# Optimization experiments

Measured on AMD Instinct MI355X. Metric: run time of the kernel, lower is better.

Reference implementation:

```python
import jax, jax.numpy as jnp
import numpy as np

IN_FEATURES = 16080
TREES = 64
LEAVES = 128
CLASSES = 16
BATCH = 64


def setup_inputs() -> dict:
    key = jax.random.key(0)
    k_x, k_w, k_b, k_c = jax.random.split(key, 4)
    x = jax.random.normal(k_x, (BATCH, TREES, IN_FEATURES), dtype=jnp.float32)
    # nn.Linear(16080, leaves): weight [leaves, in], bias [leaves]
    lim = 1.0 / np.sqrt(IN_FEATURES)
    W = jax.random.uniform(k_w, (LEAVES, IN_FEATURES), minval=-lim, maxval=lim, dtype=jnp.float32)
    b = jax.random.uniform(k_b, (LEAVES,), minval=-lim, maxval=lim, dtype=jnp.float32)
    # contribution parameter ~ U(-1, 1), shape [trees, leaves, classes]
    contribution = jax.random.uniform(k_c, (TREES, LEAVES, CLASSES), minval=-1.0, maxval=1.0, dtype=jnp.float32)
    return {"x": x, "W": W, "b": b, "contribution": contribution}


def reference(x, W, b, contribution):
    # Linear + Hardtanh: [B, T, L]
    symbolic_paths = jnp.clip(jnp.einsum('bti,li->btl', x, W) + b, -1.0, 1.0)
    # Fused form of the per-(tree,leaf) outer-product loop: [B, T, L, C]
    class_value = symbolic_paths[..., None] * contribution[None]
    p = jax.nn.softmax(class_value, axis=-1)
    # 1 - sum(p^2) over classes (Gini-style impurity): [B, T, L]
    class_value = jnp.sum(1.0 - p * p, axis=-1)
    return (symbolic_paths, class_value)
```

## Files before the change

kernel.cpp:

```cpp
#include <hip/hip_runtime.h>
#include <hip/hip_bf16.h>
#include <stdint.h>

#define IN_F   16080
#define NTREES 64
#define NLEAF  128
#define NCLS   16
#define NBATCH 64
#define M_TOT  (NBATCH*NTREES)
#define OUT_HALF (M_TOT*NLEAF)

#define BM 64
#define BN 128
#define BK 64
#define KSPLIT 16
#define NSTEPS ((IN_F + BK - 1)/BK)
#define NMBLK  (M_TOT / BM)

typedef __attribute__((ext_vector_type(8))) short short8;
typedef __attribute__((ext_vector_type(4))) float f32x4;

typedef const __attribute__((address_space(1))) uint32_t gu32_t;
typedef __attribute__((address_space(3))) uint32_t su32_t;

__device__ __forceinline__ short8 cvt8(float4 lo, float4 hi){
  union { short8 s8; __hip_bfloat162 h2[4]; } u;
  u.h2[0] = __float22bfloat162_rn(make_float2(lo.x, lo.y));
  u.h2[1] = __float22bfloat162_rn(make_float2(lo.z, lo.w));
  u.h2[2] = __float22bfloat162_rn(make_float2(hi.x, hi.y));
  u.h2[3] = __float22bfloat162_rn(make_float2(hi.z, hi.w));
  return u.s8;
}

__global__ __launch_bounds__(256)
void wcvt_kernel(const float* __restrict__ W, short* __restrict__ Wb,
                 uint32_t* __restrict__ zp){
  if (blockIdx.x == 0 && threadIdx.x < 64) zp[threadIdx.x] = 0u;
  int i = (blockIdx.x * 256 + threadIdx.x) << 3;
  float4 a = *(const float4*)(W + i);
  float4 b = *(const float4*)(W + i + 4);
  *(short8*)(Wb + i) = cvt8(a, b);
}

__global__ __launch_bounds__(256, 4)
void gemm_slab_kernel(const float* __restrict__ X,
                      const short* __restrict__ Wb,
                      float* __restrict__ slabs,
                      const short* __restrict__ zeropage){
  __shared__ __align__(16) short BsH[2][NLEAF * BK];

  const int tid = threadIdx.x;
  const int m0  = blockIdx.x * BM;
  const int kc  = blockIdx.y;
  const int s0  = (kc * NSTEPS) / KSPLIT;
  const int s1  = ((kc + 1) * NSTEPS) / KSPLIT;

  const int lane = tid & 63;
  const int wv   = tid >> 6;
  const int fr   = lane & 15;
  const int fq   = lane >> 4;

  f32x4 acc[8];
  #pragma unroll
  for (int nt = 0; nt < 8; ++nt) acc[nt] = (f32x4){0.f,0.f,0.f,0.f};

  float4 av[2][2];
  const float* arow = X + (size_t)(m0 + wv*16 + fr) * IN_F;

  {
    const int k0 = s0 * BK;
    #pragma unroll
    for (int j = 0; j < 4; ++j){
      int lin = j*256 + tid;
      int r   = lin >> 3;
      int c   = (lin & 7) ^ (r & 7);
      int gk  = k0 + (c << 3);
      const short* gp = (gk + 8 <= IN_F) ? (Wb + (size_t)r * IN_F + gk)
                                         : zeropage;
      __builtin_amdgcn_global_load_lds((gu32_t*)gp, (su32_t*)(&BsH[0][0] + lin*8),
                                       16, 0, 0);
    }
    #pragma unroll
    for (int h = 0; h < 2; ++h)
      #pragma unroll
      for (int q = 0; q < 2; ++q){
        int gk = k0 + h*32 + fq*8 + q*4;
        av[h][q] = (gk + 4 <= IN_F) ? *(const float4*)(arow + gk)
                                    : make_float4(0.f,0.f,0.f,0.f);
      }
  }

  for (int s = s0; s < s1; ++s){
    const int par = (s - s0) & 1;
    short* bcur = &BsH[par][0];
    short* bnxt = &BsH[par ^ 1][0];

    {
      const int k1 = (s + 1) * BK;
      #pragma unroll
      for (int j = 0; j < 4; ++j){
        int lin = j*256 + tid;
        int r   = lin >> 3;
        int c   = (lin & 7) ^ (r & 7);
        int gk  = k1 + (c << 3);
        const short* gp = (gk + 8 <= IN_F) ? (Wb + (size_t)r * IN_F + gk)
                                           : zeropage;
        __builtin_amdgcn_global_load_lds((gu32_t*)gp, (su32_t*)(bnxt + lin*8),
                                         16, 0, 0);
      }
    }

    asm volatile("s_waitcnt vmcnt(4)" ::: "memory");
    __builtin_amdgcn_s_barrier();

    short8 af[2];
    #pragma unroll
    for (int h = 0; h < 2; ++h)
      af[h] = cvt8(av[h][0], av[h][1]);

    {
      const int k1 = (s + 1) * BK;
      #pragma unroll
      for (int h = 0; h < 2; ++h)
        #pragma unroll
        for (int q = 0; q < 2; ++q){
          int gk = k1 + h*32 + fq*8 + q*4;
          av[h][q] = (gk + 4 <= IN_F) ? *(const float4*)(arow + gk)
                                      : make_float4(0.f,0.f,0.f,0.f);
        }
    }

    #pragma unroll
    for (int nt = 0; nt < 8; ++nt){
      const int l  = nt*16 + fr;
      const int xw = l & 7;
      const short* rowb = bcur + l*BK;
      #pragma unroll
      for (int h = 0; h < 2; ++h){
        int cc = (((h << 2) + fq) ^ xw) << 3;
        short8 bf = *(const short8*)(rowb + cc);
        acc[nt] = __builtin_amdgcn_mfma_f32_16x16x32_bf16(
                      af[h], bf, acc[nt], 0, 0, 0);
      }
    }

    __builtin_amdgcn_s_barrier();
  }

  const int rbase = m0 + wv*16 + fq*4;
  #pragma unroll
  for (int nt = 0; nt < 8; ++nt){
    int col = nt*16 + fr;
    #pragma unroll
    for (int r = 0; r < 4; ++r)
      slabs[(size_t)kc * OUT_HALF + (size_t)(rbase + r) * NLEAF + col]
          = acc[nt][r];
  }
}

__global__ __launch_bounds__(256)
void epilogue_slab_kernel(const float* __restrict__ slabs,
                          float* __restrict__ out,
                          const float* __restrict__ bias,
                          const float* __restrict__ contrib){
  int idx = blockIdx.x * 256 + threadIdx.x;
  int l   = idx & (NLEAF - 1);
  int row = idx >> 7;
  int t   = row & (NTREES - 1);

  float s = 0.f;
  #pragma unroll
  for (int kc = 0; kc < KSPLIT; ++kc)
    s += slabs[(size_t)kc * OUT_HALF + idx];
  s += bias[l];
  s = fminf(1.f, fmaxf(-1.f, s));
  out[idx] = s;

  const float4* cp = (const float4*)(contrib + (((size_t)t * NLEAF + l) << 4));
  float4 c0 = cp[0], c1 = cp[1], c2 = cp[2], c3 = cp[3];
  float v[16] = { s*c0.x, s*c0.y, s*c0.z, s*c0.w,
                  s*c1.x, s*c1.y, s*c1.z, s*c1.w,
                  s*c2.x, s*c2.y, s*c2.z, s*c2.w,
                  s*c3.x, s*c3.y, s*c3.z, s*c3.w };
  float m = v[0];
  #pragma unroll
  for (int c = 1; c < 16; ++c) m = fmaxf(m, v[c]);
  float se = 0.f, se2 = 0.f;
  #pragma unroll
  for (int c = 0; c < 16; ++c){
    float e = __expf(v[c] - m);
    se  += e;
    se2 += e * e;
  }
  out[OUT_HALF + idx] = (float)NCLS - se2 / (se * se);
}

__global__ __launch_bounds__(256, 4)
void gemm_atomic_kernel(const float* __restrict__ X,
                        const float* __restrict__ Wg,
                        float* __restrict__ accbuf,
                        const float* __restrict__ zeropage){
  __shared__ __align__(16) float BsF[BN * BK];

  const int tid = threadIdx.x;
  const int m0  = blockIdx.x * BM;
  const int kc  = blockIdx.y;
  const int s0  = (kc * NSTEPS) / KSPLIT;
  const int s1  = ((kc + 1) * NSTEPS) / KSPLIT;

  const int lane = tid & 63;
  const int wv   = tid >> 6;
  const int wm   = wv & 1;
  const int wn   = wv >> 1;
  const int fr   = lane & 15;
  const int fq   = lane >> 4;

  f32x4 acc[2][4];
  #pragma unroll
  for (int mt = 0; mt < 2; ++mt)
    #pragma unroll
    for (int nt = 0; nt < 4; ++nt) acc[mt][nt] = (f32x4){0.f,0.f,0.f,0.f};

  for (int s = s0; s < s1; ++s){
    const int k0 = s * BK;
    __syncthreads();

    float4 av[2][2][2];
    #pragma unroll
    for (int mt = 0; mt < 2; ++mt){
      const float* rowp = X + (size_t)(m0 + wm*32 + mt*16 + fr) * IN_F;
      #pragma unroll
      for (int h = 0; h < 2; ++h)
        #pragma unroll
        for (int q = 0; q < 2; ++q){
          int gk = k0 + h*32 + fq*8 + q*4;
          av[mt][h][q] = (gk + 4 <= IN_F) ? *(const float4*)(rowp + gk)
                                          : make_float4(0.f,0.f,0.f,0.f);
        }
    }

    #pragma unroll
    for (int j = 0; j < 8; ++j){
      int lin = j*256 + tid;
      int r   = lin >> 4;
      int p   = lin & 15;
      int c   = p ^ (r & 7);
      int gk  = k0 + c*4;
      const float* gp = (gk + 4 <= IN_F) ? (Wg + (size_t)r * IN_F + gk)
                                         : zeropage;
      __builtin_amdgcn_global_load_lds((gu32_t*)gp, (su32_t*)(BsF + lin*4),
                                       16, 0, 0);
    }

    short8 af[2][2];
    #pragma unroll
    for (int mt = 0; mt < 2; ++mt)
      #pragma unroll
      for (int h = 0; h < 2; ++h)
        af[mt][h] = cvt8(av[mt][h][0], av[mt][h][1]);

    __syncthreads();

    #pragma unroll
    for (int nt = 0; nt < 4; ++nt){
      const int l  = wn*64 + nt*16 + fr;
      const int xw = l & 7;
      const float* rowb = BsF + l*64;
      #pragma unroll
      for (int h = 0; h < 2; ++h){
        int c0 = h*8 + fq*2;
        float4 b0 = *(const float4*)(rowb + ((c0    ) ^ xw)*4);
        float4 b1 = *(const float4*)(rowb + ((c0 + 1) ^ xw)*4);
        short8 bf = cvt8(b0, b1);
        #pragma unroll
        for (int mt = 0; mt < 2; ++mt)
          acc[mt][nt] = __builtin_amdgcn_mfma_f32_16x16x32_bf16(
                            af[mt][h], bf, acc[mt][nt], 0, 0, 0);
      }
    }
  }

  #pragma unroll
  for (int mt = 0; mt < 2; ++mt){
    const int rbase = m0 + wm*32 + mt*16 + fq*4;
    #pragma unroll
    for (int nt = 0; nt < 4; ++nt){
      int col = wn*64 + nt*16 + fr;
      #pragma unroll
      for (int r = 0; r < 4; ++r)
        atomicAdd(&accbuf[(size_t)(rbase + r) * NLEAF + col], acc[mt][nt][r]);
    }
  }
}

__global__ __launch_bounds__(256)
void epilogue_inplace_kernel(float* __restrict__ out,
                             const float* __restrict__ bias,
                             const float* __restrict__ contrib){
  int idx = blockIdx.x * 256 + threadIdx.x;
  int l   = idx & (NLEAF - 1);
  int row = idx >> 7;
  int t   = row & (NTREES - 1);

  float s = out[idx] + bias[l];
  s = fminf(1.f, fmaxf(-1.f, s));
  out[idx] = s;

  const float4* cp = (const float4*)(contrib + (((size_t)t * NLEAF + l) << 4));
  float4 c0 = cp[0], c1 = cp[1], c2 = cp[2], c3 = cp[3];
  float v[16] = { s*c0.x, s*c0.y, s*c0.z, s*c0.w,
                  s*c1.x, s*c1.y, s*c1.z, s*c1.w,
                  s*c2.x, s*c2.y, s*c2.z, s*c2.w,
                  s*c3.x, s*c3.y, s*c3.z, s*c3.w };
  float m = v[0];
  #pragma unroll
  for (int c = 1; c < 16; ++c) m = fmaxf(m, v[c]);
  float se = 0.f, se2 = 0.f;
  #pragma unroll
  for (int c = 0; c < 16; ++c){
    float e = __expf(v[c] - m);
    se  += e;
    se2 += e * e;
  }
  out[OUT_HALF + idx] = (float)NCLS - se2 / (se * se);
}

extern "C" void kernel_launch(void* const* d_in, const int* in_sizes, int n_in,
                              void* d_out, int out_size, void* d_ws, size_t ws_size,
                              hipStream_t stream){
  const float* X       = (const float*)d_in[0];
  const float* Wg      = (const float*)d_in[1];
  const float* bias    = (const float*)d_in[2];
  const float* contrib = (const float*)d_in[3];
  float* out = (float*)d_out;

  const size_t SLAB_BYTES = (size_t)KSPLIT * OUT_HALF * sizeof(float);
  const size_t WB_BYTES   = (size_t)NLEAF * IN_F * sizeof(short);
  char* ws = (char*)d_ws;
  const int WCVT_BLOCKS = (NLEAF * IN_F) / (256 * 8);

  dim3 g1(NMBLK, KSPLIT);

  if (ws_size >= SLAB_BYTES + WB_BYTES + 256){
    float* slabs = (float*)ws;
    short* Wb    = (short*)(ws + SLAB_BYTES);
    short* zp    = (short*)(ws + SLAB_BYTES + WB_BYTES);
    wcvt_kernel<<<WCVT_BLOCKS, 256, 0, stream>>>(Wg, Wb, (uint32_t*)zp);
    gemm_slab_kernel<<<g1, 256, 0, stream>>>(X, Wb, slabs, zp);
    epilogue_slab_kernel<<<OUT_HALF / 256, 256, 0, stream>>>(slabs, out, bias, contrib);
  } else {
    hipMemsetAsync(out, 0, (size_t)OUT_HALF * sizeof(float), stream);
    hipMemsetAsync(ws, 0, 256, stream);
    gemm_atomic_kernel<<<g1, 256, 0, stream>>>(X, Wg, out, (const float*)ws);
    epilogue_inplace_kernel<<<OUT_HALF / 256, 256, 0, stream>>>(out, bias, contrib);
  }
}
```

Measured before the change: 393.5 us.

## Load bf16 weight fragments directly into registers, dropping the LDS staging

The GEMM kernel no longer stages W tiles through shared memory with global_load_lds and barriers. Each lane now loads its MFMA B fragments straight from global memory into registers, double-buffered across the two K halves. The converted weight buffer is padded to a K stride of 16192 with zero fill, which removes the zero-page bounds handling on B loads. The aim is to cut LDS traffic and barrier stalls, but each of the four waves now fetches the same B data separately through L2 and needs more registers.

Result: slower. 518.5 us (+31.8%).

```diff
diff --git a/kernel.cpp b/kernel.cpp
--- a/kernel.cpp
+++ b/kernel.cpp
@@ -11,11 +11,11 @@
 #define OUT_HALF (M_TOT*NLEAF)
 
 #define BM 64
-#define BN 128
 #define BK 64
 #define KSPLIT 16
 #define NSTEPS ((IN_F + BK - 1)/BK)
 #define NMBLK  (M_TOT / BM)
+#define WB_K   16192
 
 typedef __attribute__((ext_vector_type(8))) short short8;
 typedef __attribute__((ext_vector_type(4))) float f32x4;
@@ -33,22 +33,26 @@
 }
 
 __global__ __launch_bounds__(256)
-void wcvt_kernel(const float* __restrict__ W, short* __restrict__ Wb,
-                 uint32_t* __restrict__ zp){
-  if (blockIdx.x == 0 && threadIdx.x < 64) zp[threadIdx.x] = 0u;
-  int i = (blockIdx.x * 256 + threadIdx.x) << 3;
-  float4 a = *(const float4*)(W + i);
-  float4 b = *(const float4*)(W + i + 4);
-  *(short8*)(Wb + i) = cvt8(a, b);
+void wcvt_kernel(const float* __restrict__ W, short* __restrict__ Wb){
+  const int r = blockIdx.x;
+  const float* src = W  + (size_t)r * IN_F;
+  short*       dst = Wb + (size_t)r * WB_K;
+  for (int i = threadIdx.x * 8; i < WB_K; i += 256 * 8){
+    if (i + 8 <= IN_F){
+      float4 a = *(const float4*)(src + i);
+      float4 b = *(const float4*)(src + i + 4);
+      *(short8*)(dst + i) = cvt8(a, b);
+    } else {
+      short8 z = {0,0,0,0,0,0,0,0};
+      *(short8*)(dst + i) = z;
+    }
+  }
 }
 
 __global__ __launch_bounds__(256, 4)
-void gemm_slab_kernel(const float* __restrict__ X,
-                      const short* __restrict__ Wb,
-                      float* __restrict__ slabs,
-                      const short* __restrict__ zeropage){
-  __shared__ __align__(16) short BsH[2][NLEAF * BK];
-
+void gemm_reg_kernel(const float* __restrict__ X,
+                     const short* __restrict__ Wb,
+                     float* __restrict__ slabs){
   const int tid = threadIdx.x;
   const int m0  = blockIdx.x * BM;
   const int kc  = blockIdx.y;
@@ -64,88 +68,55 @@
   #pragma unroll
   for (int nt = 0; nt < 8; ++nt) acc[nt] = (f32x4){0.f,0.f,0.f,0.f};
 
+  const float* arow = X  + (size_t)(m0 + wv*16 + fr) * IN_F;
+  const short* brow = Wb + (size_t)fr * WB_K + fq*8;
+
   float4 av[2][2];
-  const float* arow = X + (size_t)(m0 + wv*16 + fr) * IN_F;
-
-  {
-    const int k0 = s0 * BK;
-    #pragma unroll
-    for (int j = 0; j < 4; ++j){
-      int lin = j*256 + tid;
-      int r   = lin >> 3;
-      int c   = (lin & 7) ^ (r & 7);
-      int gk  = k0 + (c << 3);
-      const short* gp = (gk + 8 <= IN_F) ? (Wb + (size_t)r * IN_F + gk)
-                                         : zeropage;
-      __builtin_amdgcn_global_load_lds((gu32_t*)gp, (su32_t*)(&BsH[0][0] + lin*8),
-                                       16, 0, 0);
-    }
-    #pragma unroll
-    for (int h = 0; h < 2; ++h)
-      #pragma unroll
-      for (int q = 0; q < 2; ++q){
-        int gk = k0 + h*32 + fq*8 + q*4;
-        av[h][q] = (gk + 4 <= IN_F) ? *(const float4*)(arow + gk)
-                                    : make_float4(0.f,0.f,0.f,0.f);
-      }
-  }
+  short8 b0[8], b1[8];
+
+  #define LOAD_A(s_)                                                        \
+    {                                                                       \
+      const int kk = (s_) * BK;                                             \
+      _Pragma("unroll")                                                     \
+      for (int h = 0; h < 2; ++h)                                           \
+        _Pragma("unroll")                                                   \
+        for (int q = 0; q < 2; ++q){                                        \
+          int gk = kk + h*32 + fq*8 + q*4;                                  \
+          bool ok = (gk + 4 <= IN_F);                                       \
+          float4 vv = *(const float4*)(arow + (ok ? gk : 0));               \
+          av[h][q] = ok ? vv : make_float4(0.f,0.f,0.f,0.f);                \
+        }                                                                   \
+    }
+
+  #define LOAD_B(dst_, s_, h_)                                              \
+    {                                                                       \
+      const short* bp = brow + (s_) * BK + (h_) * 32;                       \
+      _Pragma("unroll")                                                     \
+      for (int nt = 0; nt < 8; ++nt)                                        \
+        dst_[nt] = *(const short8*)(bp + (size_t)nt * (16 * WB_K));         \
+    }
+
+  LOAD_B(b0, s0, 0)
+  LOAD_B(b1, s0, 1)
+  LOAD_A(s0)
 
   for (int s = s0; s < s1; ++s){
-    const int par = (s - s0) & 1;
-    short* bcur = &BsH[par][0];
-    short* bnxt = &BsH[par ^ 1][0];
-
-    {
-      const int k1 = (s + 1) * BK;
-      #pragma unroll
-      for (int j = 0; j < 4; ++j){
-        int lin = j*256 + tid;
-        int r   = lin >> 3;
-        int c   = (lin & 7) ^ (r & 7);
-        int gk  = k1 + (c << 3);
-        const short* gp = (gk + 8 <= IN_F) ? (Wb + (size_t)r * IN_F + gk)
-                                           : zeropage;
-        __builtin_amdgcn_global_load_lds((gu32_t*)gp, (su32_t*)(bnxt + lin*8),
-                                         16, 0, 0);
-      }
-    }
-
-    asm volatile("s_waitcnt vmcnt(4)" ::: "memory");
-    __builtin_amdgcn_s_barrier();
-
-    short8 af[2];
-    #pragma unroll
-    for (int h = 0; h < 2; ++h)
-      af[h] = cvt8(av[h][0], av[h][1]);
-
-    {
-      const int k1 = (s + 1) * BK;
-      #pragma unroll
-      for (int h = 0; h < 2; ++h)
-        #pragma unroll
-        for (int q = 0; q < 2; ++q){
-          int gk = k1 + h*32 + fq*8 + q*4;
-          av[h][q] = (gk + 4 <= IN_F) ? *(const float4*)(arow + gk)
-                                      : make_float4(0.f,0.f,0.f,0.f);
-        }
-    }
-
-    #pragma unroll
-    for (int nt = 0; nt < 8; ++nt){
-      const int l  = nt*16 + fr;
-      const int xw = l & 7;
-      const short* rowb = bcur + l*BK;
-      #pragma unroll
-      for (int h = 0; h < 2; ++h){
-        int cc = (((h << 2) + fq) ^ xw) << 3;
-        short8 bf = *(const short8*)(rowb + cc);
-        acc[nt] = __builtin_amdgcn_mfma_f32_16x16x32_bf16(
-                      af[h], bf, acc[nt], 0, 0, 0);
-      }
-    }
-
-    __builtin_amdgcn_s_barrier();
-  }
+    short8 af0 = cvt8(av[0][0], av[0][1]);
+    short8 af1 = cvt8(av[1][0], av[1][1]);
+    LOAD_A(s + 1)
+
+    #pragma unroll
+    for (int nt = 0; nt < 8; ++nt)
+      acc[nt] = __builtin_amdgcn_mfma_f32_16x16x32_bf16(af0, b0[nt], acc[nt], 0, 0, 0);
+    LOAD_B(b0, s + 1, 0)
+
+    #pragma unroll
+    for (int nt = 0; nt < 8; ++nt)
+      acc[nt] = __builtin_amdgcn_mfma_f32_16x16x32_bf16(af1, b1[nt], acc[nt], 0, 0, 0);
+    LOAD_B(b1, s + 1, 1)
+  }
+  #undef LOAD_A
+  #undef LOAD_B
 
   const int rbase = m0 + wv*16 + fq*4;
   #pragma unroll
@@ -200,7 +171,7 @@
                         const float* __restrict__ Wg,
                         float* __restrict__ accbuf,
                         const float* __restrict__ zeropage){
-  __shared__ __align__(16) float BsF[BN * BK];
+  __shared__ __align__(16) float BsF[NLEAF * BK];
 
   const int tid = threadIdx.x;
   const int m0  = blockIdx.x * BM;
@@ -335,18 +306,16 @@
   float* out = (float*)d_out;
 
   const size_t SLAB_BYTES = (size_t)KSPLIT * OUT_HALF * sizeof(float);
-  const size_t WB_BYTES   = (size_t)NLEAF * IN_F * sizeof(short);
+  const size_t WB_BYTES   = (size_t)NLEAF * WB_K * sizeof(short);
   char* ws = (char*)d_ws;
-  const int WCVT_BLOCKS = (NLEAF * IN_F) / (256 * 8);
 
   dim3 g1(NMBLK, KSPLIT);
 
-  if (ws_size >= SLAB_BYTES + WB_BYTES + 256){
+  if (ws_size >= SLAB_BYTES + WB_BYTES){
     float* slabs = (float*)ws;
     short* Wb    = (short*)(ws + SLAB_BYTES);
-    short* zp    = (short*)(ws + SLAB_BYTES + WB_BYTES);
-    wcvt_kernel<<<WCVT_BLOCKS, 256, 0, stream>>>(Wg, Wb, (uint32_t*)zp);
-    gemm_slab_kernel<<<g1, 256, 0, stream>>>(X, Wb, slabs, zp);
+    wcvt_kernel<<<NLEAF, 256, 0, stream>>>(Wg, Wb);
+    gemm_reg_kernel<<<g1, 256, 0, stream>>>(X, Wb, slabs);
     epilogue_slab_kernel<<<OUT_HALF / 256, 256, 0, stream>>>(slabs, out, bias, contrib);
   } else {
     hipMemsetAsync(out, 0, (size_t)OUT_HALF * sizeof(float), stream);
```
